# Kernel tuning notes

Measured on AMD Instinct MI355X. Metric: run time of the kernel, lower is better.

Reference implementation:

```python
import jax, jax.numpy as jnp
import numpy as np

DIM = 768
NUM_HEADS = 12
HEAD_DIM = DIM // NUM_HEADS
SCALE = HEAD_DIM ** -0.5


def setup_inputs() -> dict:
    key = jax.random.key(0)
    ks = jax.random.split(key, 8)
    B, Nx, Ny = 4, 1024, 2048
    std = DIM ** -0.5
    return {
        "x": jax.random.normal(ks[0], (B, Nx, DIM), dtype=jnp.float32),
        "y": jax.random.normal(ks[1], (B, Ny, DIM), dtype=jnp.float32),
        "Wq": jax.random.normal(ks[2], (DIM, DIM), dtype=jnp.float32) * std,
        "Wk": jax.random.normal(ks[3], (DIM, DIM), dtype=jnp.float32) * std,
        "Wv": jax.random.normal(ks[4], (DIM, DIM), dtype=jnp.float32) * std,
        "Wproj": jax.random.normal(ks[5], (DIM, DIM), dtype=jnp.float32) * std,
        "bproj": jnp.zeros((DIM,), dtype=jnp.float32),
    }


def reference(x, y, Wq, Wk, Wv, Wproj, bproj):
    B, Nx, C = x.shape
    Ny = y.shape[1]
    H, D = NUM_HEADS, HEAD_DIM
    # Linear projections (torch nn.Linear: x @ W.T), then split heads -> [B,H,N,D]
    q = (x @ Wq.T).reshape(B, Nx, H, D).transpose(0, 2, 1, 3)
    k = (y @ Wk.T).reshape(B, Ny, H, D).transpose(0, 2, 1, 3)
    v = (y @ Wv.T).reshape(B, Ny, H, D).transpose(0, 2, 1, 3)
    # Manual attention: full [B,H,Nx,Ny] score matrix (faithful to source)
    attn = jnp.einsum("bhqd,bhkd->bhqk", q, k) * SCALE
    attn = jax.nn.softmax(attn, axis=-1)
    out = jnp.einsum("bhqk,bhkd->bhqd", attn, v)
    out = out.transpose(0, 2, 1, 3).reshape(B, Nx, C)
    return out @ Wproj.T + bproj
```

## Files before the change

### kernel.cpp

```cpp
#include <hip/hip_runtime.h>
#include <hip/hip_bf16.h>

typedef unsigned short u16;
typedef __attribute__((ext_vector_type(8))) short bf16x8;
typedef __attribute__((ext_vector_type(4))) float f32x4;
typedef __attribute__((ext_vector_type(16))) float f32x16;
typedef __attribute__((ext_vector_type(4))) unsigned u32x4;

#define MFMA(a, b, c) __builtin_amdgcn_mfma_f32_16x16x32_bf16(a, b, c, 0, 0, 0)
#define MFMA32(a, b, c) __builtin_amdgcn_mfma_f32_32x32x16_bf16(a, b, c, 0, 0, 0)

#define STAGE16(g, l) __builtin_amdgcn_global_load_lds( \
    (const __attribute__((address_space(1))) void*)(g),  \
    (__attribute__((address_space(3))) void*)(l), 16, 0, 0)

__device__ __forceinline__ u16 f2bf(float f) {
  union { float f; unsigned u; } v; v.f = f;
  return (u16)((v.u + 0x7fffu + ((v.u >> 16) & 1u)) >> 16);
}

__device__ __forceinline__ unsigned pack_bf2(float lo, float hi) {
  __hip_bfloat162 h = __float22bfloat162_rn(float2{lo, hi});
  return *reinterpret_cast<unsigned*>(&h);
}

__device__ __forceinline__ void pl32swap(unsigned &a, unsigned &b) {
  asm("v_permlane32_swap_b32 %0, %1" : "+v"(a), "+v"(b));
}

__global__ __launch_bounds__(256) void convert_all(
    const float* __restrict__ x, const float* __restrict__ y,
    const float* __restrict__ wq, const float* __restrict__ wk,
    const float* __restrict__ wv, const float* __restrict__ wp,
    u16* __restrict__ xb, u16* __restrict__ yb,
    u16* __restrict__ wqb, u16* __restrict__ wkb,
    u16* __restrict__ wvb, u16* __restrict__ wpb)
{
  constexpr int G0 = 4096 * 768 / 4;
  constexpr int G1 = G0 + 8192 * 768 / 4;
  constexpr int GW = 768 * 768 / 4;
  int g = blockIdx.x * 256 + threadIdx.x;
  const float* s; u16* d; int o;
  if      (g < G0)          { s = x;  d = xb;  o = g; }
  else if (g < G1)          { s = y;  d = yb;  o = g - G0; }
  else if (g < G1 + GW)     { s = wq; d = wqb; o = g - G1; }
  else if (g < G1 + 2*GW)   { s = wk; d = wkb; o = g - G1 - GW; }
  else if (g < G1 + 3*GW)   { s = wv; d = wvb; o = g - G1 - 2*GW; }
  else if (g < G1 + 4*GW)   { s = wp; d = wpb; o = g - G1 - 3*GW; }
  else return;
  float4 v = reinterpret_cast<const float4*>(s)[o];
  ushort4 r;
  r.x = f2bf(v.x); r.y = f2bf(v.y); r.z = f2bf(v.z); r.w = f2bf(v.w);
  reinterpret_cast<ushort4*>(d)[o] = r;
}

template <bool PROJ>
__global__ __launch_bounds__(256) void gemm_k(
    const u16* __restrict__ A0, const u16* __restrict__ A1,
    const u16* __restrict__ W0, const u16* __restrict__ W1,
    const u16* __restrict__ W2,
    u16* __restrict__ Qb, u16* __restrict__ Kb, u16* __restrict__ Vw,
    const float* __restrict__ bias, float* __restrict__ fout)
{
  __shared__ u16 sA[128 * 64];
  __shared__ u16 sB[128 * 64];

  const int nper = PROJ ? 24 : 120;
  int bid = (blockIdx.x & 7) * nper + (blockIdx.x >> 3);

  const u16 *A, *W;
  int mode, mt, nt;
  if (PROJ)           { mode = 3; A = A0; W = W0; mt = bid / 6;        nt = bid % 6; }
  else if (bid < 192) { mode = 0; A = A0; W = W0; mt = bid / 6;        nt = bid % 6; }
  else if (bid < 576) { mode = 1; A = A1; W = W1; mt = (bid-192) / 6;  nt = (bid-192) % 6; }
  else                { mode = 2; A = A1; W = W2; mt = (bid-576) / 6;  nt = (bid-576) % 6; }

  const int tid = threadIdx.x;
  const int w = tid >> 6, l = tid & 63;
  const int wm = w >> 1, wn = w & 1;
  const int g = l >> 4, m = l & 15;

  const int mbase = mt * 128, nbase = nt * 128;

  const int srow = l >> 3;
  const int schunk = ((l & 7) ^ srow) * 8;
  const u16* Ag = A + (size_t)(mbase + srow) * 768 + schunk;
  const u16* Wg = W + (size_t)(nbase + srow) * 768 + schunk;

  f32x4 acc[4][4] = {};

  for (int kt = 0; kt < 12; ++kt) {
    __syncthreads();
    const int ko = kt * 64;
#pragma unroll
    for (int i = 0; i < 4; ++i) {
      const int ri = (i * 4 + w) * 8;
      STAGE16(Ag + (size_t)ri * 768 + ko, (char*)sA + ri * 128);
      STAGE16(Wg + (size_t)ri * 768 + ko, (char*)sB + ri * 128);
    }
    __syncthreads();

    bf16x8 af[2][4], bfr[2][4];
#pragma unroll
    for (int c = 0; c < 2; ++c)
#pragma unroll
      for (int t = 0; t < 4; ++t) {
        const int ar = wm * 64 + t * 16 + m;
        const int br = wn * 64 + t * 16 + m;
        const int cp = ((c * 4 + g) ^ (l & 7)) * 16;
        af[c][t]  = *reinterpret_cast<const bf16x8*>((const char*)sA + ar * 128 + cp);
        bfr[c][t] = *reinterpret_cast<const bf16x8*>((const char*)sB + br * 128 + cp);
      }
#pragma unroll
    for (int c = 0; c < 2; ++c)
#pragma unroll
      for (int mi = 0; mi < 4; ++mi)
#pragma unroll
        for (int ni = 0; ni < 4; ++ni)
          acc[mi][ni] = MFMA(af[c][mi], bfr[c][ni], acc[mi][ni]);
  }

  const float QSCALE = 0.18033688011112042f;
  const int rowb = mbase + wm * 64 + g * 4;
  const int colb = nbase + wn * 64 + m;
#pragma unroll
  for (int mi = 0; mi < 4; ++mi) {
#pragma unroll
    for (int ni = 0; ni < 4; ++ni) {
      const int col = colb + ni * 16;
      const int h = col >> 6, d = col & 63;
      if constexpr (PROJ) {
#pragma unroll
        for (int r = 0; r < 4; ++r) {
          const int row = rowb + mi * 16 + r;
          fout[(size_t)row * 768 + col] = acc[mi][ni][r] + bias[col];
        }
      } else {
        if (mode == 0) {
#pragma unroll
          for (int r = 0; r < 4; ++r) {
            const int row = rowb + mi * 16 + r;
            const int b_ = row >> 10, n = row & 1023;
            Qb[((size_t)(b_ * 12 + h) * 1024 + n) * 64 + d] =
                f2bf(acc[mi][ni][r] * QSCALE);
          }
        } else if (mode == 1) {
#pragma unroll
          for (int r = 0; r < 4; ++r) {
            const int row = rowb + mi * 16 + r;
            const int b_ = row >> 11, n = row & 2047;
            Kb[((size_t)(b_ * 12 + h) * 2048 + n) * 64 + d] = f2bf(acc[mi][ni][r]);
          }
        } else {
          const int row = rowb + mi * 16;
          const int b_ = row >> 11, n = row & 2047;
          ushort4 pk;
          pk.x = f2bf(acc[mi][ni][0]); pk.y = f2bf(acc[mi][ni][1]);
          pk.z = f2bf(acc[mi][ni][2]); pk.w = f2bf(acc[mi][ni][3]);
          *reinterpret_cast<ushort4*>(
              Vw + (size_t)(b_ * 12 + h) * 131072 + (n >> 3) * 512 + d * 8 + (n & 7)) = pk;
        }
      }
    }
  }
}

__global__ __launch_bounds__(256) void attn_fwd(
    const u16* __restrict__ Qb, const u16* __restrict__ Kb,
    const u16* __restrict__ Vw, u16* __restrict__ AOb)
{
  __shared__ u16 sK[2][2][64 * 64];

  const int bid = blockIdx.x;
  const int bh = bid % 48, qt = bid / 48;
  const int tid = threadIdx.x;
  const int w = tid >> 6, l = tid & 63;
  const int h = l >> 5, q = l & 31;
  const int qw = w & 1, half = w >> 1;

  const u16* Kbh = Kb + ((size_t)bh * 2048 + half * 1024) * 64;
  const u16* Vbh = Vw + (size_t)bh * 131072 + (size_t)half * 128 * 512
                      + h * 512 + q * 8;

  const int q0 = qt * 64 + qw * 32;
  const u16* qp = Qb + ((size_t)bh * 1024 + q0 + q) * 64 + 8 * h;
  bf16x8 qf[4];
#pragma unroll
  for (int t = 0; t < 4; ++t)
    qf[t] = *reinterpret_cast<const bf16x8*>(qp + 16 * t);

  const int srow = l >> 3;
  const int soff = ((l & 7) ^ srow) * 8;
  const int rg = qw * 32;

  bf16x8 ones;
#pragma unroll
  for (int i = 0; i < 8; ++i) ones[i] = (short)0x3F80;

  f32x16 o0 = {}, o1 = {}, la = {};

#pragma unroll
  for (int i = 0; i < 4; ++i)
    STAGE16(Kbh + (size_t)(rg + i * 8 + srow) * 64 + soff,
            (char*)&sK[half][0][0] + (rg + i * 8) * 128);

  int cur = 0;
  for (int kt = 0; kt < 16; ++kt) {
    __syncthreads();

    if (kt < 15) {
#pragma unroll
      for (int i = 0; i < 4; ++i)
        STAGE16(Kbh + (size_t)((kt + 1) * 64 + rg + i * 8 + srow) * 64 + soff,
                (char*)&sK[half][cur ^ 1][0] + (rg + i * 8) * 128);
    }

    const u16* vb = Vbh + (size_t)(kt * 8) * 512;
    bf16x8 vf0[4], vf1[4];
#pragma unroll
    for (int t = 0; t < 4; ++t) {
      vf0[t] = *reinterpret_cast<const bf16x8*>(vb + t * 1024);
      vf1[t] = *reinterpret_cast<const bf16x8*>(vb + t * 1024 + 256);
    }

    const char* sKc = (const char*)&sK[half][cur][0];
    f32x16 s0 = {}, s1 = {};
    __builtin_amdgcn_s_setprio(1);
#pragma unroll
    for (int t = 0; t < 4; ++t) {
      const int pc = ((2 * t + h) ^ (q & 7)) * 16;
      const bf16x8 k0 = *reinterpret_cast<const bf16x8*>(sKc + q * 128 + pc);
      const bf16x8 k1 = *reinterpret_cast<const bf16x8*>(sKc + (q + 32) * 128 + pc);
      s0 = MFMA32(k0, qf[t], s0);
      s1 = MFMA32(k1, qf[t], s1);
    }
    __builtin_amdgcn_s_setprio(0);

    float p0[16], p1[16];
#pragma unroll
    for (int r = 0; r < 16; ++r) p0[r] = exp2f(s0[r]);
#pragma unroll
    for (int r = 0; r < 16; ++r) p1[r] = exp2f(s1[r]);

    unsigned pk[2][4][2];
#pragma unroll
    for (int qd = 0; qd < 4; ++qd) {
      pk[0][qd][0] = pack_bf2(p0[4*qd+0], p0[4*qd+1]);
      pk[0][qd][1] = pack_bf2(p0[4*qd+2], p0[4*qd+3]);
      pk[1][qd][0] = pack_bf2(p1[4*qd+0], p1[4*qd+1]);
      pk[1][qd][1] = pack_bf2(p1[4*qd+2], p1[4*qd+3]);
    }

    __builtin_amdgcn_s_setprio(1);
#pragma unroll
    for (int t = 0; t < 4; ++t) {
      const int c = t >> 1, j0 = 2 * (t & 1);
      unsigned x0 = pk[c][j0][0], y0 = pk[c][j0 + 1][0];
      unsigned x1 = pk[c][j0][1], y1 = pk[c][j0 + 1][1];
      pl32swap(x0, y0);
      pl32swap(x1, y1);
      u32x4 fv; fv[0] = x0; fv[1] = x1; fv[2] = y0; fv[3] = y1;
      const bf16x8 af = __builtin_bit_cast(bf16x8, fv);
      o0 = MFMA32(af, vf0[t], o0);
      o1 = MFMA32(af, vf1[t], o1);
      la = MFMA32(af, ones, la);
    }
    __builtin_amdgcn_s_setprio(0);
    cur ^= 1;
  }

  __syncthreads();
  float* buf = (float*)&sK[0][0][0];
  float* bp_ = buf + (size_t)(qw * 48) * 64 + l;
  if (half == 1) {
#pragma unroll
    for (int r = 0; r < 16; ++r) {
      bp_[r * 64]        = o0[r];
      bp_[(16 + r) * 64] = o1[r];
      bp_[(32 + r) * 64] = la[r];
    }
  }
  __syncthreads();
  if (half == 0) {
    const int b_ = bh / 12, hd = bh % 12;
#pragma unroll
    for (int r = 0; r < 16; ++r) {
      const float ot0 = o0[r] + bp_[r * 64];
      const float ot1 = o1[r] + bp_[(16 + r) * 64];
      const float lt  = la[r] + bp_[(32 + r) * 64];
      const float rl = 1.f / lt;
      const int row = q0 + (r >> 2) * 8 + 4 * h + (r & 3);
      u16* dst = AOb + ((size_t)b_ * 1024 + row) * 768 + hd * 64 + q;
      dst[0]  = f2bf(ot0 * rl);
      dst[32] = f2bf(ot1 * rl);
    }
  }
}

extern "C" void kernel_launch(void* const* d_in, const int* in_sizes, int n_in,
                              void* d_out, int out_size, void* d_ws, size_t ws_size,
                              hipStream_t stream)
{
  const float* x  = (const float*)d_in[0];
  const float* y  = (const float*)d_in[1];
  const float* wq = (const float*)d_in[2];
  const float* wk = (const float*)d_in[3];
  const float* wv = (const float*)d_in[4];
  const float* wp = (const float*)d_in[5];
  const float* bp = (const float*)d_in[6];
  float* out = (float*)d_out;

  char* ws = (char*)d_ws;
  u16* xb  = (u16*)ws; ws += (size_t)4096 * 768 * 2;
  u16* yb  = (u16*)ws; ws += (size_t)8192 * 768 * 2;
  u16* wqb = (u16*)ws; ws += (size_t)768 * 768 * 2;
  u16* wkb = (u16*)ws; ws += (size_t)768 * 768 * 2;
  u16* wvb = (u16*)ws; ws += (size_t)768 * 768 * 2;
  u16* wpb = (u16*)ws; ws += (size_t)768 * 768 * 2;
  u16* Qb  = (u16*)ws; ws += (size_t)4096 * 768 * 2;
  u16* Kb  = (u16*)ws; ws += (size_t)8192 * 768 * 2;
  u16* Vw  = (u16*)ws; ws += (size_t)8192 * 768 * 2;
  u16* AOb = (u16*)ws; ws += (size_t)4096 * 768 * 2;

  convert_all<<<11520, 256, 0, stream>>>(x, y, wq, wk, wv, wp,
                                         xb, yb, wqb, wkb, wvb, wpb);
  gemm_k<false><<<960, 256, 0, stream>>>(xb, yb, wqb, wkb, wvb,
                                         Qb, Kb, Vw, nullptr, nullptr);
  attn_fwd<<<768, 256, 0, stream>>>(Qb, Kb, Vw, AOb);
  gemm_k<true><<<192, 256, 0, stream>>>(AOb, nullptr, wpb, nullptr, nullptr,
                                        nullptr, nullptr, nullptr, bp, out);
}
```

Measured before the change: 125.1 us.

## Store Q/K in MFMA-fragment layout and load K directly from global in attention

The projection GEMM now writes Q and K in a pre-swizzled fragment layout, so the attention kernel can load K fragments straight from global memory as contiguous 16-byte vectors instead of staging them through double-buffered LDS. The attention block shrinks to 128 threads (2 waves splitting the key range, 32 queries per block) with twice as many blocks. The row-sum MFMA against a ones vector is replaced by scalar adds plus a cross-lane shuffle. This removes the LDS staging and barriers in the main loop, but relies on global/L2 bandwidth and latency hiding for K reads, and the scattered 2-byte writes in the GEMM epilogue may cost more.

Result: faster. 116.0 us (-7.3%).

```diff
diff --git a/kernel.cpp b/kernel.cpp
--- a/kernel.cpp
+++ b/kernel.cpp
@@ -59,7 +59,7 @@
     const u16* __restrict__ A0, const u16* __restrict__ A1,
     const u16* __restrict__ W0, const u16* __restrict__ W1,
     const u16* __restrict__ W2,
-    u16* __restrict__ Qb, u16* __restrict__ Kb, u16* __restrict__ Vw,
+    u16* __restrict__ Qa, u16* __restrict__ Ka, u16* __restrict__ Vw,
     const float* __restrict__ bias, float* __restrict__ fout)
 {
   __shared__ u16 sA[128 * 64];
@@ -129,6 +129,8 @@
     for (int ni = 0; ni < 4; ++ni) {
       const int col = colb + ni * 16;
       const int h = col >> 6, d = col & 63;
+      const int t_ = d >> 4, hh = (d >> 3) & 1, di = d & 7;
+      const int fo = t_ * 512 + hh * 256 + di;
       if constexpr (PROJ) {
 #pragma unroll
         for (int r = 0; r < 4; ++r) {
@@ -141,7 +143,7 @@
           for (int r = 0; r < 4; ++r) {
             const int row = rowb + mi * 16 + r;
             const int b_ = row >> 10, n = row & 1023;
-            Qb[((size_t)(b_ * 12 + h) * 1024 + n) * 64 + d] =
+            Qa[((size_t)(b_ * 12 + h) * 32 + (n >> 5)) * 2048 + fo + (n & 31) * 8] =
                 f2bf(acc[mi][ni][r] * QSCALE);
           }
         } else if (mode == 1) {
@@ -149,7 +151,8 @@
           for (int r = 0; r < 4; ++r) {
             const int row = rowb + mi * 16 + r;
             const int b_ = row >> 11, n = row & 2047;
-            Kb[((size_t)(b_ * 12 + h) * 2048 + n) * 64 + d] = f2bf(acc[mi][ni][r]);
+            Ka[(size_t)(b_ * 12 + h) * 131072 + (n >> 5) * 2048 + fo + (n & 31) * 8] =
+                f2bf(acc[mi][ni][r]);
           }
         } else {
           const int row = rowb + mi * 16;
@@ -165,82 +168,71 @@
   }
 }
 
-__global__ __launch_bounds__(256) void attn_fwd(
-    const u16* __restrict__ Qb, const u16* __restrict__ Kb,
+__global__ __launch_bounds__(128, 3) void attn_fwd(
+    const u16* __restrict__ Qa, const u16* __restrict__ Ka,
     const u16* __restrict__ Vw, u16* __restrict__ AOb)
 {
-  __shared__ u16 sK[2][2][64 * 64];
+  __shared__ float cO[32 * 64];
+  __shared__ float cL[2][32];
 
   const int bid = blockIdx.x;
   const int bh = bid % 48, qt = bid / 48;
   const int tid = threadIdx.x;
   const int w = tid >> 6, l = tid & 63;
   const int h = l >> 5, q = l & 31;
-  const int qw = w & 1, half = w >> 1;
-
-  const u16* Kbh = Kb + ((size_t)bh * 2048 + half * 1024) * 64;
-  const u16* Vbh = Vw + (size_t)bh * 131072 + (size_t)half * 128 * 512
-                      + h * 512 + q * 8;
-
-  const int q0 = qt * 64 + qw * 32;
-  const u16* qp = Qb + ((size_t)bh * 1024 + q0 + q) * 64 + 8 * h;
+
+  const u16* qb = Qa + (size_t)(bh * 32 + qt) * 2048 + h * 256 + q * 8;
   bf16x8 qf[4];
 #pragma unroll
   for (int t = 0; t < 4; ++t)
-    qf[t] = *reinterpret_cast<const bf16x8*>(qp + 16 * t);
-
-  const int srow = l >> 3;
-  const int soff = ((l & 7) ^ srow) * 8;
-  const int rg = qw * 32;
-
-  bf16x8 ones;
-#pragma unroll
-  for (int i = 0; i < 8; ++i) ones[i] = (short)0x3F80;
-
-  f32x16 o0 = {}, o1 = {}, la = {};
-
-#pragma unroll
-  for (int i = 0; i < 4; ++i)
-    STAGE16(Kbh + (size_t)(rg + i * 8 + srow) * 64 + soff,
-            (char*)&sK[half][0][0] + (rg + i * 8) * 128);
-
-  int cur = 0;
+    qf[t] = *reinterpret_cast<const bf16x8*>(qb + t * 512);
+
+  const u16* kb = Ka + (size_t)bh * 131072 + (size_t)w * 65536 + h * 256 + q * 8;
+  const u16* vb = Vw + (size_t)bh * 131072 + (size_t)w * 65536 + h * 512 + q * 8;
+
+  f32x16 o0 = {}, o1 = {};
+  float lrun = 0.f;
+
   for (int kt = 0; kt < 16; ++kt) {
-    __syncthreads();
-
-    if (kt < 15) {
-#pragma unroll
-      for (int i = 0; i < 4; ++i)
-        STAGE16(Kbh + (size_t)((kt + 1) * 64 + rg + i * 8 + srow) * 64 + soff,
-                (char*)&sK[half][cur ^ 1][0] + (rg + i * 8) * 128);
-    }
-
-    const u16* vb = Vbh + (size_t)(kt * 8) * 512;
-    bf16x8 vf0[4], vf1[4];
+    const u16* kp = kb + kt * 4096;
+    const u16* vp = vb + kt * 4096;
+
+    bf16x8 kf0[4], kf1[4];
 #pragma unroll
     for (int t = 0; t < 4; ++t) {
-      vf0[t] = *reinterpret_cast<const bf16x8*>(vb + t * 1024);
-      vf1[t] = *reinterpret_cast<const bf16x8*>(vb + t * 1024 + 256);
-    }
-
-    const char* sKc = (const char*)&sK[half][cur][0];
+      kf0[t] = *reinterpret_cast<const bf16x8*>(kp + t * 512);
+      kf1[t] = *reinterpret_cast<const bf16x8*>(kp + 2048 + t * 512);
+    }
+
     f32x16 s0 = {}, s1 = {};
     __builtin_amdgcn_s_setprio(1);
 #pragma unroll
     for (int t = 0; t < 4; ++t) {
-      const int pc = ((2 * t + h) ^ (q & 7)) * 16;
-      const bf16x8 k0 = *reinterpret_cast<const bf16x8*>(sKc + q * 128 + pc);
-      const bf16x8 k1 = *reinterpret_cast<const bf16x8*>(sKc + (q + 32) * 128 + pc);
-      s0 = MFMA32(k0, qf[t], s0);
-      s1 = MFMA32(k1, qf[t], s1);
+      s0 = MFMA32(kf0[t], qf[t], s0);
+      s1 = MFMA32(kf1[t], qf[t], s1);
     }
     __builtin_amdgcn_s_setprio(0);
 
+    bf16x8 vf0[4], vf1[4];
+#pragma unroll
+    for (int t = 0; t < 4; ++t) {
+      vf0[t] = *reinterpret_cast<const bf16x8*>(vp + t * 1024);
+      vf1[t] = *reinterpret_cast<const bf16x8*>(vp + t * 1024 + 256);
+    }
+
     float p0[16], p1[16];
 #pragma unroll
     for (int r = 0; r < 16; ++r) p0[r] = exp2f(s0[r]);
 #pragma unroll
     for (int r = 0; r < 16; ++r) p1[r] = exp2f(s1[r]);
+
+    float a8[8];
+#pragma unroll
+    for (int i = 0; i < 8; ++i)
+      a8[i] = (p0[2*i] + p0[2*i+1]) + (p1[2*i] + p1[2*i+1]);
+    float ts = ((a8[0]+a8[1]) + (a8[2]+a8[3])) + ((a8[4]+a8[5]) + (a8[6]+a8[7]));
+    ts += __shfl_xor(ts, 32);
+    lrun += ts;
 
     unsigned pk[2][4][2];
 #pragma unroll
@@ -263,34 +255,32 @@
       const bf16x8 af = __builtin_bit_cast(bf16x8, fv);
       o0 = MFMA32(af, vf0[t], o0);
       o1 = MFMA32(af, vf1[t], o1);
-      la = MFMA32(af, ones, la);
     }
     __builtin_amdgcn_s_setprio(0);
-    cur ^= 1;
-  }
-
+  }
+
+  if (w == 1) {
+    if (h == 0) cL[1][q] = lrun;
+#pragma unroll
+    for (int r = 0; r < 16; ++r) {
+      const int crow = (r >> 2) * 8 + 4 * h + (r & 3);
+      cO[crow * 64 + q]      = o0[r];
+      cO[crow * 64 + 32 + q] = o1[r];
+    }
+  } else {
+    if (h == 0) cL[0][q] = lrun;
+  }
   __syncthreads();
-  float* buf = (float*)&sK[0][0][0];
-  float* bp_ = buf + (size_t)(qw * 48) * 64 + l;
-  if (half == 1) {
+  if (w == 0) {
+    const int b_ = bh / 12, hd = bh % 12;
 #pragma unroll
     for (int r = 0; r < 16; ++r) {
-      bp_[r * 64]        = o0[r];
-      bp_[(16 + r) * 64] = o1[r];
-      bp_[(32 + r) * 64] = la[r];
-    }
-  }
-  __syncthreads();
-  if (half == 0) {
-    const int b_ = bh / 12, hd = bh % 12;
-#pragma unroll
-    for (int r = 0; r < 16; ++r) {
-      const float ot0 = o0[r] + bp_[r * 64];
-      const float ot1 = o1[r] + bp_[(16 + r) * 64];
-      const float lt  = la[r] + bp_[(32 + r) * 64];
+      const int crow = (r >> 2) * 8 + 4 * h + (r & 3);
+      const float lt = cL[0][crow] + cL[1][crow];
       const float rl = 1.f / lt;
-      const int row = q0 + (r >> 2) * 8 + 4 * h + (r & 3);
-      u16* dst = AOb + ((size_t)b_ * 1024 + row) * 768 + hd * 64 + q;
+      const float ot0 = o0[r] + cO[crow * 64 + q];
+      const float ot1 = o1[r] + cO[crow * 64 + 32 + q];
+      u16* dst = AOb + ((size_t)b_ * 1024 + qt * 32 + crow) * 768 + hd * 64 + q;
       dst[0]  = f2bf(ot0 * rl);
       dst[32] = f2bf(ot1 * rl);
     }
@@ -317,16 +307,16 @@
   u16* wkb = (u16*)ws; ws += (size_t)768 * 768 * 2;
   u16* wvb = (u16*)ws; ws += (size_t)768 * 768 * 2;
   u16* wpb = (u16*)ws; ws += (size_t)768 * 768 * 2;
-  u16* Qb  = (u16*)ws; ws += (size_t)4096 * 768 * 2;
-  u16* Kb  = (u16*)ws; ws += (size_t)8192 * 768 * 2;
+  u16* Qa  = (u16*)ws; ws += (size_t)4096 * 768 * 2;
+  u16* Ka  = (u16*)ws; ws += (size_t)8192 * 768 * 2;
   u16* Vw  = (u16*)ws; ws += (size_t)8192 * 768 * 2;
   u16* AOb = (u16*)ws; ws += (size_t)4096 * 768 * 2;
 
   convert_all<<<11520, 256, 0, stream>>>(x, y, wq, wk, wv, wp,
                                          xb, yb, wqb, wkb, wvb, wpb);
   gemm_k<false><<<960, 256, 0, stream>>>(xb, yb, wqb, wkb, wvb,
-                                         Qb, Kb, Vw, nullptr, nullptr);
-  attn_fwd<<<768, 256, 0, stream>>>(Qb, Kb, Vw, AOb);
+                                         Qa, Ka, Vw, nullptr, nullptr);
+  attn_fwd<<<1536, 128, 0, stream>>>(Qa, Ka, Vw, AOb);
   gemm_k<true><<<192, 256, 0, stream>>>(AOb, nullptr, wpb, nullptr, nullptr,
                                         nullptr, nullptr, nullptr, bp, out);
 }
```
